# Performance work log

Measured on AMD Instinct MI355X. Metric: run time of the kernel, lower is better.

The kernel has to match this reference:

```python
import jax, jax.numpy as jnp
import numpy as np

K = 20  # neighbors per point (module default)


def _knn_idx(x, k):
    # x: [N, d] -> indices of k nearest points (self included, as in torch_cluster.knn)
    d2 = jnp.sum(x * x, axis=-1)
    dist = d2[:, None] + d2[None, :] - 2.0 * (x @ x.T)  # [N, N] squared distances
    _, idx = jax.lax.top_k(-dist, k)  # smallest distances
    return idx  # [N, k]


def _mlp(h, layers):
    # layers: list of (W, b, relu_flag); BN is identity (eval mode, fresh running stats)
    for W, b, relu in layers:
        h = h @ W + b
        if relu:
            h = jax.nn.relu(h)
    return h


def _dynamic_edge_conv(x, layers, k=K):
    # x: [B, N, d]; dynamic kNN graph per graph, edge feat [x_i, x_j - x_i], MLP, max-aggr
    idx = jax.vmap(lambda xx: _knn_idx(jax.lax.stop_gradient(xx), k))(x)  # [B, N, k]
    xj = jax.vmap(lambda xx, ii: xx[ii])(x, idx)  # [B, N, k, d] neighbor gather
    xi = x[:, :, None, :]
    feat = jnp.concatenate([jnp.broadcast_to(xi, xj.shape), xj - xi], axis=-1)  # [B,N,k,2d]
    return jnp.max(_mlp(feat, layers), axis=2)  # [B, N, d_out]


def setup_inputs() -> dict:
    key = jax.random.key(0)
    ks = jax.random.split(key, 20)
    s = 0.05
    B, N, PD, OUT = 8, 4096, 2, 10
    f32 = jnp.float32

    def w(k, shape):
        return jax.random.normal(k, shape, dtype=f32) * s

    return {
        "data": jax.random.normal(ks[0], (B, N, PD), dtype=f32),
        # conv1 MLP: [2*PD, 64, 64, 64]
        "c1w1": w(ks[1], (2 * PD, 64)), "c1b1": jnp.zeros((64,), f32),
        "c1w2": w(ks[2], (64, 64)),     "c1b2": jnp.zeros((64,), f32),
        "c1w3": w(ks[3], (64, 64)),     "c1b3": jnp.zeros((64,), f32),
        # conv2 MLP: [2*64, 128]
        "c2w1": w(ks[4], (128, 128)),   "c2b1": jnp.zeros((128,), f32),
        # lin1: 192 -> 1024
        "lin1_w": w(ks[5], (192, 1024)), "lin1_b": jnp.zeros((1024,), f32),
        # head MLP: [1024, 512, 256, OUT]
        "mw1": w(ks[6], (1024, 512)), "mb1": jnp.zeros((512,), f32),
        "mw2": w(ks[7], (512, 256)),  "mb2": jnp.zeros((256,), f32),
        "mw3": w(ks[8], (256, OUT)),  "mb3": jnp.zeros((OUT,), f32),
    }


def reference(data, c1w1, c1b1, c1w2, c1b2, c1w3, c1b3, c2w1, c2b1,
              lin1_w, lin1_b, mw1, mb1, mw2, mb2, mw3, mb3):
    # DynamicEdgeConv 1: MLP([4,64,64,64]) (plain last layer)
    x1 = _dynamic_edge_conv(data, [(c1w1, c1b1, True), (c1w2, c1b2, True), (c1w3, c1b3, False)])
    # DynamicEdgeConv 2: MLP([128,128]) (single plain linear)
    x2 = _dynamic_edge_conv(x1, [(c2w1, c2b1, False)])
    out = jnp.concatenate([x1, x2], axis=-1) @ lin1_w + lin1_b  # [B, N, 1024]
    out = jnp.max(out, axis=1)  # global max pool over points -> [B, 1024]
    out = _mlp(out, [(mw1, mb1, True), (mw2, mb2, True), (mw3, mb3, False)])
    return jax.nn.log_softmax(out, axis=1)
```

## Files before the change

kernel.cpp:

```cpp
#include <hip/hip_runtime.h>
#include <math.h>

#define DEVI static __device__ __forceinline__
#define F_INF __builtin_inff()

DEVI bool lexlt(float d, int i, float dr, int ir)
{
    return (d < dr) || (d == dr && i < ir);
}

DEVI void insert20(float* bd, int* bi, float d, int i)
{
#pragma unroll
    for (int j = 19; j >= 1; --j) {
        bool lt  = d < bd[j];
        bool ltp = d < bd[j - 1];
        float nd = ltp ? bd[j - 1] : d;
        int   ni = ltp ? bi[j - 1] : i;
        bd[j] = lt ? nd : bd[j];
        bi[j] = lt ? ni : bi[j];
    }
    bool lt0 = d < bd[0];
    bd[0] = lt0 ? d : bd[0];
    bi[0] = lt0 ? i : bi[0];
}

DEVI void insert_tiered(float* bd, int* bi, float d, int i)
{
    if (__all(!(d < bd[15]))) {
#pragma unroll
        for (int j = 19; j >= 17; --j) {
            bool lt  = d < bd[j];
            bool ltp = d < bd[j - 1];
            float nd = ltp ? bd[j - 1] : d;
            int   ni = ltp ? bi[j - 1] : i;
            bd[j] = lt ? nd : bd[j];
            bi[j] = lt ? ni : bi[j];
        }
        bool lt16 = d < bd[16];
        bd[16] = lt16 ? d : bd[16];
        bi[16] = lt16 ? i : bi[16];
    } else if (__all(!(d < bd[7]))) {
#pragma unroll
        for (int j = 19; j >= 9; --j) {
            bool lt  = d < bd[j];
            bool ltp = d < bd[j - 1];
            float nd = ltp ? bd[j - 1] : d;
            int   ni = ltp ? bi[j - 1] : i;
            bd[j] = lt ? nd : bd[j];
            bi[j] = lt ? ni : bi[j];
        }
        bool lt8 = d < bd[8];
        bd[8] = lt8 ? d : bd[8];
        bi[8] = lt8 ? i : bi[8];
    } else {
        insert20(bd, bi, d, i);
    }
}

DEVI void flushT(float* bd, int* bi, float d, int i, int e, int cnt)
{
    bool want = (e < cnt) && (d < bd[19]);
    if (__any(want))
        insert_tiered(bd, bi, want ? d : F_INF, want ? i : 0x7FFFFFFF);
}

#define FLUSH() do { \
    flushT(bd, bi, a0, j0, 0, cnt); \
    flushT(bd, bi, a1, j1, 1, cnt); \
    flushT(bd, bi, a2, j2, 2, cnt); \
    flushT(bd, bi, a3, j3, 3, cnt); \
    cnt = 0; thr = bd[19]; \
} while (0)

#define APPEND(dv, civ) do { \
    bool pass_ = (dv) < thr; \
    if (pass_) { \
        a0 = (cnt == 0) ? (dv) : a0; j0 = (cnt == 0) ? (civ) : j0; \
        a1 = (cnt == 1) ? (dv) : a1; j1 = (cnt == 1) ? (civ) : j1; \
        a2 = (cnt == 2) ? (dv) : a2; j2 = (cnt == 2) ? (civ) : j2; \
        a3 = (cnt == 3) ? (dv) : a3; j3 = (cnt == 3) ? (civ) : j3; \
        ++cnt; \
    } \
    if (__any(cnt == 4)) { FLUSH(); } \
} while (0)

__global__ __launch_bounds__(256) void k_merge8(const float* __restrict__ partD,
                                                const int* __restrict__ partI,
                                                int* __restrict__ idxo)
{
    int q = blockIdx.x * 256 + threadIdx.x;
    const float* rd = partD + (size_t)q * 160;
    const int*   ri = partI + (size_t)q * 160;
    int p0 = 0, p1 = 0, p2 = 0, p3 = 0, p4 = 0, p5 = 0, p6 = 0, p7 = 0;
    int* op = idxo + (size_t)q * 20;
    for (int r = 0; r < 20; ++r) {
        float d0 = rd[p0],        d1 = rd[20 + p1];
        float d2v = rd[40 + p2],  d3 = rd[60 + p3];
        float d4 = rd[80 + p4],   d5 = rd[100 + p5];
        float d6 = rd[120 + p6],  d7 = rd[140 + p7];
        int   i0 = ri[p0],        i1 = ri[20 + p1];
        int   i2 = ri[40 + p2],   i3 = ri[60 + p3];
        int   i4v = ri[80 + p4],  i5 = ri[100 + p5];
        int   i6 = ri[120 + p6],  i7 = ri[140 + p7];
        bool wA = lexlt(d1, i1, d0, i0);   float dA = wA ? d1 : d0; int iA = wA ? i1 : i0; int sA = wA ? 1 : 0;
        bool wB = lexlt(d3, i3, d2v, i2);  float dB = wB ? d3 : d2v; int iB = wB ? i3 : i2; int sB = wB ? 3 : 2;
        bool wC = lexlt(d5, i5, d4, i4v);  float dC = wC ? d5 : d4; int iC = wC ? i5 : i4v; int sC = wC ? 5 : 4;
        bool wD = lexlt(d7, i7, d6, i6);   float dD = wD ? d7 : d6; int iD = wD ? i7 : i6; int sD = wD ? 7 : 6;
        bool wE = lexlt(dB, iB, dA, iA);   float dE = wE ? dB : dA; int iE = wE ? iB : iA; int sE = wE ? sB : sA;
        bool wF = lexlt(dD, iD, dC, iC);   float dF = wF ? dD : dC; int iF = wF ? iD : iC; int sF = wF ? sD : sC;
        bool wG = lexlt(dF, iF, dE, iE);   int ig = wG ? iF : iE;   int sg = wG ? sF : sE;
        op[r] = ig;
        p0 += (sg == 0); p1 += (sg == 1); p2 += (sg == 2); p3 += (sg == 3);
        p4 += (sg == 4); p5 += (sg == 5); p6 += (sg == 6); p7 += (sg == 7);
    }
}

__global__ __launch_bounds__(256, 4) void k_knn2d(const float* __restrict__ x,
                                                  float* __restrict__ partD, int* __restrict__ partI)
{
    __shared__ float2 pts[4096];
    int t = threadIdx.x;
    int blk = blockIdx.x;
    int b = blk >> 7;
    int qt = (blk >> 1) & 63;
    int s = blk & 1;
    const float* xb = x + (size_t)b * 4096 * 2;
    for (int f = t; f < 2048; f += 256)
        ((float4*)pts)[f] = ((const float4*)xb)[f];
    __syncthreads();

    int l = t & 63, w = t >> 6;
    int q = qt * 64 + l;
    float2 qp = pts[q];
    float d2i = qp.x * qp.x + qp.y * qp.y;

    float bd[20]; int bi[20];
#pragma unroll
    for (int j = 0; j < 20; ++j) { bd[j] = F_INF; bi[j] = -1; }
    int cnt = 0; float thr = F_INF;
    float a0 = 0, a1 = 0, a2 = 0, a3 = 0;
    int   j0 = 0, j1 = 0, j2 = 0, j3 = 0;

    int m0 = s * 2048 + w * 512;
    for (int m = m0; m < m0 + 512; ++m) {
        float2 p = pts[m];
        float d2j = p.x * p.x + p.y * p.y;
        float dot = qp.x * p.x + qp.y * p.y;
        float dist = (d2i + d2j) - 2.0f * dot;
        APPEND(dist, m);
    }
    FLUSH();

    size_t base = (((size_t)(b * 4096 + q)) * 8 + s * 4 + w) * 20;
#pragma unroll
    for (int k = 0; k < 20; ++k) { partD[base + k] = bd[k]; partI[base + k] = bi[k]; }
}

__global__ void k_prep1(const float* __restrict__ x, const float* __restrict__ w1,
                        const float* __restrict__ b1, float* __restrict__ pm, float* __restrict__ qv)
{
    int tid = blockIdx.x * 256 + threadIdx.x;
    int n = tid >> 6, i = tid & 63;
    float x0 = x[(size_t)n * 2], x1v = x[(size_t)n * 2 + 1];
    float wa = w1[i], wb = w1[64 + i], wc = w1[128 + i], wd = w1[192 + i];
    pm[tid] = fmaf(x0, wa - wc, fmaf(x1v, wb - wd, b1[i]));
    qv[tid] = fmaf(x0, wc, x1v * wd);
}

__global__ __launch_bounds__(256) void k_edge1(const float* __restrict__ pm, const float* __restrict__ q,
                                               const int* __restrict__ idx1,
                                               const float* __restrict__ w2, const float* __restrict__ b2,
                                               const float* __restrict__ w3, const float* __restrict__ b3,
                                               float* __restrict__ x1, float* __restrict__ d2x1)
{
    int t = threadIdx.x;
    int w = t >> 6, l = t & 63;
    int pg = l / 20;
    int k  = l - pg * 20;
    int n0 = blockIdx.x * 12 + w * 3 + pg;
    bool valid = (l < 60) && (n0 < 32768);
    int n = valid ? n0 : 0;
    int b = n >> 12;
    int j = idx1[(size_t)n * 20 + k];
    const float4* pmr = (const float4*)(pm + (size_t)n * 64);
    const float4* qr  = (const float4*)(q + ((size_t)(b * 4096) + j) * 64);

    float h1[64];
#pragma unroll
    for (int i4 = 0; i4 < 16; ++i4) {
        float4 a = pmr[i4], c = qr[i4];
        h1[i4 * 4 + 0] = fmaxf(a.x + c.x, 0.f);
        h1[i4 * 4 + 1] = fmaxf(a.y + c.y, 0.f);
        h1[i4 * 4 + 2] = fmaxf(a.z + c.z, 0.f);
        h1[i4 * 4 + 3] = fmaxf(a.w + c.w, 0.f);
    }
    float h2[64];
#pragma unroll
    for (int o = 0; o < 64; ++o) h2[o] = b2[o];
#pragma unroll
    for (int i = 0; i < 64; ++i) {
        const float* r = w2 + i * 64;
#pragma unroll
        for (int o = 0; o < 64; ++o) h2[o] = fmaf(h1[i], r[o], h2[o]);
    }
#pragma unroll
    for (int o = 0; o < 64; ++o) h2[o] = fmaxf(h2[o], 0.f);

    float h3[64];
#pragma unroll
    for (int o = 0; o < 64; ++o) h3[o] = b3[o];
#pragma unroll
    for (int i = 0; i < 64; ++i) {
        const float* r = w3 + i * 64;
#pragma unroll
        for (int o = 0; o < 64; ++o) h3[o] = fmaf(h2[i], r[o], h3[o]);
    }

    int s16 = (k + 16 < 20) ? (l + 16) : l;
    int s8  = (k + 8  < 20) ? (l + 8)  : l;
    int s4  = (k + 4  < 20) ? (l + 4)  : l;
    int s2  = (k + 2  < 20) ? (l + 2)  : l;
    int s1  = (k + 1  < 20) ? (l + 1)  : l;
#pragma unroll
    for (int o = 0; o < 64; ++o) {
        float v = h3[o];
        v = fmaxf(v, __shfl(v, s16));
        v = fmaxf(v, __shfl(v, s8));
        v = fmaxf(v, __shfl(v, s4));
        v = fmaxf(v, __shfl(v, s2));
        v = fmaxf(v, __shfl(v, s1));
        h3[o] = v;
    }
    if (valid && k == 0) {
        float d2 = 0.f;
#pragma unroll
        for (int o = 0; o < 64; ++o) d2 += h3[o] * h3[o];
        float4* op = (float4*)(x1 + (size_t)n * 64);
#pragma unroll
        for (int i4 = 0; i4 < 16; ++i4)
            op[i4] = make_float4(h3[i4 * 4], h3[i4 * 4 + 1], h3[i4 * 4 + 2], h3[i4 * 4 + 3]);
        d2x1[n] = d2;
    }
}

#define S68 68
__global__ __launch_bounds__(256, 4) void k_knn64(const float* __restrict__ x1,
                                                  const float* __restrict__ d2x1,
                                                  float* __restrict__ partD, int* __restrict__ partI)
{
    __shared__ float smem[2 * 64 * S68 + 128];
    float* Qs   = smem;
    float* CsDs = smem + 64 * S68;
    float* d2q  = smem + 2 * 64 * S68;
    float* d2c  = d2q + 64;

    int t  = threadIdx.x;
    int blk = blockIdx.x;
    int bb = blk >> 7;
    int qt = (blk >> 1) & 63;
    int s  = blk & 1;
    int qbase  = bb * 4096 + qt * 64;
    int cstart = s * 2048;

    for (int f = t; f < 1024; f += 256) {
        int qq = f >> 4, dp = f & 15;
        *(float4*)&Qs[qq * S68 + dp * 4] =
            *(const float4*)(x1 + ((size_t)(qbase + qq)) * 64 + dp * 4);
    }
    if (t < 64) d2q[t] = d2x1[qbase + t];

    int m = t & 15, cb = t >> 4;
    int w = t >> 6, l = t & 63;

    float bd[20]; int bi[20];
#pragma unroll
    for (int j = 0; j < 20; ++j) { bd[j] = F_INF; bi[j] = -1; }
    int cnt = 0; float thr = F_INF;
    float a0 = 0, a1 = 0, a2 = 0, a3 = 0;
    int   j0 = 0, j1 = 0, j2 = 0, j3 = 0;

    float d2qr[4];
    bool first = true;

    for (int T = 0; T < 32; ++T) {
        int cbase = bb * 4096 + cstart + T * 64;
        for (int f = t; f < 1024; f += 256) {
            int cc = f >> 4, dp = f & 15;
            *(float4*)&CsDs[cc * S68 + dp * 4] =
                *(const float4*)(x1 + ((size_t)(cbase + cc)) * 64 + dp * 4);
        }
        if (t < 64) d2c[t] = d2x1[cbase + t];
        __syncthreads();
        if (first) {
#pragma unroll
            for (int i = 0; i < 4; ++i) d2qr[i] = d2q[m + 16 * i];
            first = false;
        }

        float acc[4][4];
#pragma unroll
        for (int i = 0; i < 4; ++i)
#pragma unroll
            for (int j = 0; j < 4; ++j) acc[i][j] = 0.f;
#pragma unroll
        for (int dc = 0; dc < 16; ++dc) {
            float4 qv[4], cv[4];
#pragma unroll
            for (int i = 0; i < 4; ++i) qv[i] = *(const float4*)&Qs[(m + 16 * i) * S68 + dc * 4];
#pragma unroll
            for (int j = 0; j < 4; ++j) cv[j] = *(const float4*)&CsDs[(cb + 16 * j) * S68 + dc * 4];
#pragma unroll
            for (int i = 0; i < 4; ++i)
#pragma unroll
                for (int j = 0; j < 4; ++j) {
                    acc[i][j] = fmaf(qv[i].x, cv[j].x, acc[i][j]);
                    acc[i][j] = fmaf(qv[i].y, cv[j].y, acc[i][j]);
                    acc[i][j] = fmaf(qv[i].z, cv[j].z, acc[i][j]);
                    acc[i][j] = fmaf(qv[i].w, cv[j].w, acc[i][j]);
                }
        }
        float d2cr[4];
#pragma unroll
        for (int j = 0; j < 4; ++j) d2cr[j] = d2c[cb + 16 * j];
        __syncthreads();

#pragma unroll
        for (int i = 0; i < 4; ++i)
#pragma unroll
            for (int j = 0; j < 4; ++j)
                CsDs[(m + 16 * i) * S68 + (cb + 16 * j)] =
                    (d2qr[i] + d2cr[j]) - 2.0f * acc[i][j];
        __syncthreads();

        const float4* drow = (const float4*)&CsDs[l * S68 + w * 16];
        int cib = cstart + T * 64 + w * 16;
#pragma unroll
        for (int j4 = 0; j4 < 4; ++j4) {
            float4 dv = drow[j4];
            int ci = cib + j4 * 4;
            APPEND(dv.x, ci + 0);
            APPEND(dv.y, ci + 1);
            APPEND(dv.z, ci + 2);
            APPEND(dv.w, ci + 3);
        }
        __syncthreads();
    }
    FLUSH();

    size_t base = (((size_t)(qbase + l)) * 8 + s * 4 + w) * 20;
#pragma unroll
    for (int k = 0; k < 20; ++k) { partD[base + k] = bd[k]; partI[base + k] = bi[k]; }
}

__global__ __launch_bounds__(128) void k_prep2(const float* __restrict__ x1, const float* __restrict__ w,
                                               const float* __restrict__ bias,
                                               float* __restrict__ T, float* __restrict__ V)
{
    __shared__ float xs[8][64];
    int o = threadIdx.x;
    int g = blockIdx.x * 8;
    for (int t = threadIdx.x; t < 512; t += 128) xs[t >> 6][t & 63] = x1[(size_t)g * 64 + t];
    __syncthreads();
    float at[8] = {}, av[8] = {};
    for (int i = 0; i < 64; ++i) {
        float wt = w[i * 128 + o], wv = w[(64 + i) * 128 + o];
#pragma unroll
        for (int p = 0; p < 8; ++p) {
            float xv = xs[p][i];
            at[p] = fmaf(xv, wt, at[p]);
            av[p] = fmaf(xv, wv, av[p]);
        }
    }
    float bo = bias[o];
#pragma unroll
    for (int p = 0; p < 8; ++p) {
        T[(size_t)(g + p) * 128 + o] = at[p] - av[p] + bo;
        V[(size_t)(g + p) * 128 + o] = av[p];
    }
}

__global__ __launch_bounds__(256) void k_edge2(const float* __restrict__ T, const float* __restrict__ V,
                                               const int* __restrict__ idx2, float* __restrict__ x2)
{
    int t = threadIdx.x;
    int p = t >> 5, oc = t & 31;
    int n = blockIdx.x * 8 + p;
    int b = n >> 12;
    const int* ip = idx2 + (size_t)n * 20;
    float4 mx = make_float4(-F_INF, -F_INF, -F_INF, -F_INF);
    for (int k = 0; k < 20; ++k) {
        int j = ip[k];
        float4 v = ((const float4*)(V + ((size_t)(b * 4096) + j) * 128))[oc];
        mx.x = fmaxf(mx.x, v.x); mx.y = fmaxf(mx.y, v.y);
        mx.z = fmaxf(mx.z, v.z); mx.w = fmaxf(mx.w, v.w);
    }
    float4 tv = ((const float4*)(T + (size_t)n * 128))[oc];
    float4 r = make_float4(tv.x + mx.x, tv.y + mx.y, tv.z + mx.z, tv.w + mx.w);
    ((float4*)(x2 + (size_t)n * 128))[oc] = r;
}

__global__ __launch_bounds__(256) void k_lin1max(const float* __restrict__ x1, const float* __restrict__ x2,
                                                 const float* __restrict__ w, const float* __restrict__ bias,
                                                 float* __restrict__ partial)
{
    __shared__ float fs[32][192];
    int blk = blockIdx.x;
    int b = blk >> 7, c = blk & 127;
    int base_n = b * 4096 + c * 32;
    for (int t = threadIdx.x; t < 2048; t += 256) {
        int n = t >> 6, i = t & 63;
        fs[n][i] = x1[(size_t)(base_n + n) * 64 + i];
    }
    for (int t = threadIdx.x; t < 4096; t += 256) {
        int n = t >> 7, i = t & 127;
        fs[n][64 + i] = x2[(size_t)(base_n + n) * 128 + i];
    }
    __syncthreads();

    float acc[32][4];
#pragma unroll
    for (int n = 0; n < 32; ++n)
#pragma unroll
        for (int oo = 0; oo < 4; ++oo) acc[n][oo] = 0.f;

    for (int i4 = 0; i4 < 48; ++i4) {
        float wv[4][4];
#pragma unroll
        for (int r = 0; r < 4; ++r)
#pragma unroll
            for (int oo = 0; oo < 4; ++oo)
                wv[r][oo] = w[(size_t)(i4 * 4 + r) * 1024 + oo * 256 + threadIdx.x];
#pragma unroll
        for (int n = 0; n < 32; ++n) {
            float4 f = *(const float4*)&fs[n][i4 * 4];
#pragma unroll
            for (int oo = 0; oo < 4; ++oo) {
                acc[n][oo] = fmaf(f.x, wv[0][oo], acc[n][oo]);
                acc[n][oo] = fmaf(f.y, wv[1][oo], acc[n][oo]);
                acc[n][oo] = fmaf(f.z, wv[2][oo], acc[n][oo]);
                acc[n][oo] = fmaf(f.w, wv[3][oo], acc[n][oo]);
            }
        }
    }
#pragma unroll
    for (int oo = 0; oo < 4; ++oo) {
        int o = oo * 256 + threadIdx.x;
        float m = -F_INF;
#pragma unroll
        for (int n = 0; n < 32; ++n) m = fmaxf(m, acc[n][oo]);
        partial[((size_t)b * 128 + c) * 1024 + o] = m + bias[o];
    }
}

__global__ void k_red(const float* __restrict__ partial, float* __restrict__ pooled)
{
    int t = blockIdx.x * 256 + threadIdx.x;
    int b = t >> 10, o = t & 1023;
    float m = -F_INF;
    for (int c = 0; c < 128; ++c) m = fmaxf(m, partial[((size_t)b * 128 + c) * 1024 + o]);
    pooled[t] = m;
}

__global__ __launch_bounds__(256) void k_fc1(const float* __restrict__ pooled, const float* __restrict__ w,
                                             const float* __restrict__ bias, float* __restrict__ g1)
{
    __shared__ float ps[8 * 1024];
    for (int t = threadIdx.x; t < 8192; t += 256) ps[t] = pooled[t];
    __syncthreads();
    int o = blockIdx.x * 256 + threadIdx.x;
    float acc[8] = {};
    for (int i4 = 0; i4 < 256; ++i4) {
        float w0 = w[(size_t)(i4 * 4 + 0) * 512 + o];
        float w1v = w[(size_t)(i4 * 4 + 1) * 512 + o];
        float w2v = w[(size_t)(i4 * 4 + 2) * 512 + o];
        float w3v = w[(size_t)(i4 * 4 + 3) * 512 + o];
#pragma unroll
        for (int bb = 0; bb < 8; ++bb) {
            float4 f = *(const float4*)&ps[bb * 1024 + i4 * 4];
            acc[bb] = fmaf(f.x, w0, fmaf(f.y, w1v, fmaf(f.z, w2v, fmaf(f.w, w3v, acc[bb]))));
        }
    }
    float bo = bias[o];
#pragma unroll
    for (int bb = 0; bb < 8; ++bb) g1[bb * 512 + o] = fmaxf(acc[bb] + bo, 0.f);
}

__global__ __launch_bounds__(256) void k_fc2(const float* __restrict__ g1, const float* __restrict__ w,
                                             const float* __restrict__ bias, float* __restrict__ g2)
{
    __shared__ float gs[8 * 512];
    for (int t = threadIdx.x; t < 4096; t += 256) gs[t] = g1[t];
    __syncthreads();
    int o = threadIdx.x;
    float acc[8] = {};
    for (int i4 = 0; i4 < 128; ++i4) {
        float w0 = w[(size_t)(i4 * 4 + 0) * 256 + o];
        float w1v = w[(size_t)(i4 * 4 + 1) * 256 + o];
        float w2v = w[(size_t)(i4 * 4 + 2) * 256 + o];
        float w3v = w[(size_t)(i4 * 4 + 3) * 256 + o];
#pragma unroll
        for (int bb = 0; bb < 8; ++bb) {
            float4 f = *(const float4*)&gs[bb * 512 + i4 * 4];
            acc[bb] = fmaf(f.x, w0, fmaf(f.y, w1v, fmaf(f.z, w2v, fmaf(f.w, w3v, acc[bb]))));
        }
    }
    float bo = bias[o];
#pragma unroll
    for (int bb = 0; bb < 8; ++bb) g2[bb * 256 + o] = fmaxf(acc[bb] + bo, 0.f);
}

__global__ void k_fc3sm(const float* __restrict__ g2, const float* __restrict__ w,
                        const float* __restrict__ bias, float* __restrict__ out)
{
    int t = threadIdx.x;
    int b = t >> 4, l = t & 15;
    float lg = -F_INF;
    if (l < 10) {
        float a = bias[l];
        for (int i = 0; i < 256; ++i) a = fmaf(g2[b * 256 + i], w[i * 10 + l], a);
        lg = a;
    }
    float m = lg;
    m = fmaxf(m, __shfl_xor(m, 1, 16));
    m = fmaxf(m, __shfl_xor(m, 2, 16));
    m = fmaxf(m, __shfl_xor(m, 4, 16));
    m = fmaxf(m, __shfl_xor(m, 8, 16));
    float e = (l < 10) ? expf(lg - m) : 0.f;
    float s = e;
    s += __shfl_xor(s, 1, 16);
    s += __shfl_xor(s, 2, 16);
    s += __shfl_xor(s, 4, 16);
    s += __shfl_xor(s, 8, 16);
    if (l < 10) out[b * 10 + l] = (lg - m) - logf(s);
}

extern "C" void kernel_launch(void* const* d_in, const int* in_sizes, int n_in,
                              void* d_out, int out_size, void* d_ws, size_t ws_size,
                              hipStream_t stream)
{
    (void)in_sizes; (void)n_in; (void)out_size; (void)ws_size;
    const float* data  = (const float*)d_in[0];
    const float* c1w1  = (const float*)d_in[1];
    const float* c1b1  = (const float*)d_in[2];
    const float* c1w2  = (const float*)d_in[3];
    const float* c1b2  = (const float*)d_in[4];
    const float* c1w3  = (const float*)d_in[5];
    const float* c1b3  = (const float*)d_in[6];
    const float* c2w1  = (const float*)d_in[7];
    const float* c2b1  = (const float*)d_in[8];
    const float* lin1w = (const float*)d_in[9];
    const float* lin1b = (const float*)d_in[10];
    const float* mw1   = (const float*)d_in[11];
    const float* mb1   = (const float*)d_in[12];
    const float* mw2   = (const float*)d_in[13];
    const float* mb2   = (const float*)d_in[14];
    const float* mw3   = (const float*)d_in[15];
    const float* mb3   = (const float*)d_in[16];
    float* ws  = (float*)d_ws;
    int*   wsi = (int*)d_ws;
    float* out = (float*)d_out;

    const size_t OFF_IDX1 = 0;
    const size_t OFF_IDX2 = 0;
    const size_t OFF_X1   = 655360;
    const size_t OFF_D2   = 2752512;
    const size_t OFF_PM   = 2785280;
    const size_t OFF_Q    = 4882432;
    const size_t OFF_PD   = 2785280;
    const size_t OFF_PI   = 8028160;
    const size_t OFF_T    = 2785280;
    const size_t OFF_V    = 6979584;
    const size_t OFF_X2   = 11173888;
    const size_t OFF_PART = 15368192;
    const size_t OFF_POOL = 16416768;
    const size_t OFF_G1   = 16424960;
    const size_t OFF_G2   = 16429056;

    k_knn2d<<<1024, 256, 0, stream>>>(data, ws + OFF_PD, wsi + OFF_PI);
    k_merge8<<<128, 256, 0, stream>>>(ws + OFF_PD, wsi + OFF_PI, wsi + OFF_IDX1);
    k_prep1<<<8192, 256, 0, stream>>>(data, c1w1, c1b1, ws + OFF_PM, ws + OFF_Q);
    k_edge1<<<2731, 256, 0, stream>>>(ws + OFF_PM, ws + OFF_Q, wsi + OFF_IDX1,
                                      c1w2, c1b2, c1w3, c1b3, ws + OFF_X1, ws + OFF_D2);
    k_knn64<<<1024, 256, 0, stream>>>(ws + OFF_X1, ws + OFF_D2, ws + OFF_PD, wsi + OFF_PI);
    k_merge8<<<128, 256, 0, stream>>>(ws + OFF_PD, wsi + OFF_PI, wsi + OFF_IDX2);
    k_prep2<<<4096, 128, 0, stream>>>(ws + OFF_X1, c2w1, c2b1, ws + OFF_T, ws + OFF_V);
    k_edge2<<<4096, 256, 0, stream>>>(ws + OFF_T, ws + OFF_V, wsi + OFF_IDX2, ws + OFF_X2);
    k_lin1max<<<1024, 256, 0, stream>>>(ws + OFF_X1, ws + OFF_X2, lin1w, lin1b, ws + OFF_PART);
    k_red<<<32, 256, 0, stream>>>(ws + OFF_PART, ws + OFF_POOL);
    k_fc1<<<2, 256, 0, stream>>>(ws + OFF_POOL, mw1, mb1, ws + OFF_G1);
    k_fc2<<<1, 256, 0, stream>>>(ws + OFF_G1, mw2, mb2, ws + OFF_G2);
    k_fc3sm<<<1, 128, 0, stream>>>(ws + OFF_G2, mw3, mb3, out);
}
```

Measured before the change: 1.472 ms.

## Separate candidate and distance tiles to overlap next-tile load with selection

```diff
diff --git a/kernel.cpp b/kernel.cpp
--- a/kernel.cpp
+++ b/kernel.cpp
@@ -245,15 +245,16 @@
 }
 
 #define S68 68
-__global__ __launch_bounds__(256, 4) void k_knn64(const float* __restrict__ x1,
+__global__ __launch_bounds__(256, 3) void k_knn64(const float* __restrict__ x1,
                                                   const float* __restrict__ d2x1,
                                                   float* __restrict__ partD, int* __restrict__ partI)
 {
-    __shared__ float smem[2 * 64 * S68 + 128];
-    float* Qs   = smem;
-    float* CsDs = smem + 64 * S68;
-    float* d2q  = smem + 2 * 64 * S68;
-    float* d2c  = d2q + 64;
+    __shared__ float smem[3 * 64 * S68 + 128];
+    float* Qs  = smem;
+    float* Cs  = smem + 64 * S68;
+    float* Ds  = smem + 2 * 64 * S68;
+    float* d2q = smem + 3 * 64 * S68;
+    float* d2c = d2q + 64;
 
     int t  = threadIdx.x;
     int blk = blockIdx.x;
@@ -269,6 +270,16 @@
             *(const float4*)(x1 + ((size_t)(qbase + qq)) * 64 + dp * 4);
     }
     if (t < 64) d2q[t] = d2x1[qbase + t];
+    {
+        int cbase0 = bb * 4096 + cstart;
+        for (int f = t; f < 1024; f += 256) {
+            int cc = f >> 4, dp = f & 15;
+            *(float4*)&Cs[cc * S68 + dp * 4] =
+                *(const float4*)(x1 + ((size_t)(cbase0 + cc)) * 64 + dp * 4);
+        }
+        if (t < 64) d2c[t] = d2x1[cbase0 + t];
+    }
+    __syncthreads();
 
     int m = t & 15, cb = t >> 4;
     int w = t >> 6, l = t & 63;
@@ -281,23 +292,10 @@
     int   j0 = 0, j1 = 0, j2 = 0, j3 = 0;
 
     float d2qr[4];
-    bool first = true;
+#pragma unroll
+    for (int i = 0; i < 4; ++i) d2qr[i] = d2q[m + 16 * i];
 
     for (int T = 0; T < 32; ++T) {
-        int cbase = bb * 4096 + cstart + T * 64;
-        for (int f = t; f < 1024; f += 256) {
-            int cc = f >> 4, dp = f & 15;
-            *(float4*)&CsDs[cc * S68 + dp * 4] =
-                *(const float4*)(x1 + ((size_t)(cbase + cc)) * 64 + dp * 4);
-        }
-        if (t < 64) d2c[t] = d2x1[cbase + t];
-        __syncthreads();
-        if (first) {
-#pragma unroll
-            for (int i = 0; i < 4; ++i) d2qr[i] = d2q[m + 16 * i];
-            first = false;
-        }
-
         float acc[4][4];
 #pragma unroll
         for (int i = 0; i < 4; ++i)
@@ -309,7 +307,7 @@
 #pragma unroll
             for (int i = 0; i < 4; ++i) qv[i] = *(const float4*)&Qs[(m + 16 * i) * S68 + dc * 4];
 #pragma unroll
-            for (int j = 0; j < 4; ++j) cv[j] = *(const float4*)&CsDs[(cb + 16 * j) * S68 + dc * 4];
+            for (int j = 0; j < 4; ++j) cv[j] = *(const float4*)&Cs[(cb + 16 * j) * S68 + dc * 4];
 #pragma unroll
             for (int i = 0; i < 4; ++i)
 #pragma unroll
@@ -323,17 +321,26 @@
         float d2cr[4];
 #pragma unroll
         for (int j = 0; j < 4; ++j) d2cr[j] = d2c[cb + 16 * j];
-        __syncthreads();
 
 #pragma unroll
         for (int i = 0; i < 4; ++i)
 #pragma unroll
             for (int j = 0; j < 4; ++j)
-                CsDs[(m + 16 * i) * S68 + (cb + 16 * j)] =
+                Ds[(m + 16 * i) * S68 + (cb + 16 * j)] =
                     (d2qr[i] + d2cr[j]) - 2.0f * acc[i][j];
         __syncthreads();
 
-        const float4* drow = (const float4*)&CsDs[l * S68 + w * 16];
+        if (T + 1 < 32) {
+            int cb2 = bb * 4096 + cstart + (T + 1) * 64;
+            for (int f = t; f < 1024; f += 256) {
+                int cc = f >> 4, dp = f & 15;
+                *(float4*)&Cs[cc * S68 + dp * 4] =
+                    *(const float4*)(x1 + ((size_t)(cb2 + cc)) * 64 + dp * 4);
+            }
+            if (t < 64) d2c[t] = d2x1[cb2 + t];
+        }
+
+        const float4* drow = (const float4*)&Ds[l * S68 + w * 16];
         int cib = cstart + T * 64 + w * 16;
 #pragma unroll
         for (int j4 = 0; j4 < 4; ++j4) {
```

New measurement: 1.554 ms. 1.06x slower.

## Make kNN64 candidate tiles wave-private to remove block barriers

Applied to the files above, without the earlier changes.

```diff
diff --git a/kernel.cpp b/kernel.cpp
--- a/kernel.cpp
+++ b/kernel.cpp
@@ -251,9 +251,9 @@
 {
     __shared__ float smem[2 * 64 * S68 + 128];
     float* Qs   = smem;
-    float* CsDs = smem + 64 * S68;
+    float* Cs   = smem + 64 * S68;
     float* d2q  = smem + 2 * 64 * S68;
-    float* d2c  = d2q + 64;
+    float* d2cs = d2q + 64;
 
     int t  = threadIdx.x;
     int blk = blockIdx.x;
@@ -269,9 +269,11 @@
             *(const float4*)(x1 + ((size_t)(qbase + qq)) * 64 + dp * 4);
     }
     if (t < 64) d2q[t] = d2x1[qbase + t];
-
-    int m = t & 15, cb = t >> 4;
+    __syncthreads();
+
     int w = t >> 6, l = t & 63;
+    int m = l & 15, p = l >> 4;
+    float* Crow = Cs + (16 * w) * S68;
 
     float bd[20]; int bi[20];
 #pragma unroll
@@ -281,22 +283,19 @@
     int   j0 = 0, j1 = 0, j2 = 0, j3 = 0;
 
     float d2qr[4];
-    bool first = true;
+#pragma unroll
+    for (int i = 0; i < 4; ++i) d2qr[i] = d2q[m + 16 * i];
 
     for (int T = 0; T < 32; ++T) {
-        int cbase = bb * 4096 + cstart + T * 64;
-        for (int f = t; f < 1024; f += 256) {
-            int cc = f >> 4, dp = f & 15;
-            *(float4*)&CsDs[cc * S68 + dp * 4] =
-                *(const float4*)(x1 + ((size_t)(cbase + cc)) * 64 + dp * 4);
-        }
-        if (t < 64) d2c[t] = d2x1[cbase + t];
-        __syncthreads();
-        if (first) {
-#pragma unroll
-            for (int i = 0; i < 4; ++i) d2qr[i] = d2q[m + 16 * i];
-            first = false;
-        }
+        int cg = bb * 4096 + cstart + T * 64 + 16 * w;
+
+#pragma unroll
+        for (int r = 0; r < 4; ++r) {
+            int rl = 4 * r + p;
+            *(float4*)&Crow[rl * S68 + m * 4] =
+                *(const float4*)(x1 + ((size_t)(cg + rl)) * 64 + m * 4);
+        }
+        if (l < 16) d2cs[16 * w + l] = d2x1[cg + l];
 
         float acc[4][4];
 #pragma unroll
@@ -309,7 +308,7 @@
 #pragma unroll
             for (int i = 0; i < 4; ++i) qv[i] = *(const float4*)&Qs[(m + 16 * i) * S68 + dc * 4];
 #pragma unroll
-            for (int j = 0; j < 4; ++j) cv[j] = *(const float4*)&CsDs[(cb + 16 * j) * S68 + dc * 4];
+            for (int j = 0; j < 4; ++j) cv[j] = *(const float4*)&Crow[(4 * p + j) * S68 + dc * 4];
 #pragma unroll
             for (int i = 0; i < 4; ++i)
 #pragma unroll
@@ -322,29 +321,21 @@
         }
         float d2cr[4];
 #pragma unroll
-        for (int j = 0; j < 4; ++j) d2cr[j] = d2c[cb + 16 * j];
-        __syncthreads();
-
-#pragma unroll
-        for (int i = 0; i < 4; ++i)
-#pragma unroll
-            for (int j = 0; j < 4; ++j)
-                CsDs[(m + 16 * i) * S68 + (cb + 16 * j)] =
+        for (int j = 0; j < 4; ++j) d2cr[j] = d2cs[16 * w + 4 * p + j];
+
+#pragma unroll
+        for (int j = 0; j < 4; ++j)
+#pragma unroll
+            for (int i = 0; i < 4; ++i)
+                Crow[(4 * p + j) * S68 + (m + 16 * i)] =
                     (d2qr[i] + d2cr[j]) - 2.0f * acc[i][j];
-        __syncthreads();
-
-        const float4* drow = (const float4*)&CsDs[l * S68 + w * 16];
-        int cib = cstart + T * 64 + w * 16;
-#pragma unroll
-        for (int j4 = 0; j4 < 4; ++j4) {
-            float4 dv = drow[j4];
-            int ci = cib + j4 * 4;
-            APPEND(dv.x, ci + 0);
-            APPEND(dv.y, ci + 1);
-            APPEND(dv.z, ci + 2);
-            APPEND(dv.w, ci + 3);
-        }
-        __syncthreads();
+
+        int cib = cstart + T * 64 + 16 * w;
+#pragma unroll
+        for (int c = 0; c < 16; ++c) {
+            float dv = Crow[c * S68 + l];
+            APPEND(dv, cib + c);
+        }
     }
     FLUSH();
 
```

New measurement: 1.445 ms. About the same (-1.8%).
